# Optimization experiments

Hardware: AMD Instinct MI355X
Metric: run time of the kernel (lower is better)

The kernel has to match this reference:

```python
import jax, jax.numpy as jnp
import numpy as np

B, T, D_MODEL, D_HEAD = 16, 2048, 512, 64
LAMBDA_0 = 1.0      # inverse tracker init: A_0 = I / lambda_0
FIXED_LAMBDA = 1.0  # PenaltyBuilder with fixed_lambda: u_t = sqrt(lambda) * k_t


def setup_inputs() -> dict:
    key = jax.random.key(0)
    ks = jax.random.split(key, 9)
    s_in = 1.0 / np.sqrt(D_MODEL)
    s_out = 1.0 / np.sqrt(D_HEAD)
    return {
        "x": jax.random.normal(ks[0], (B, T, D_MODEL), jnp.float32),
        "W_q": jax.random.normal(ks[1], (D_HEAD, D_MODEL), jnp.float32) * s_in,
        "b_q": jnp.zeros((D_HEAD,), jnp.float32),
        "W_k": jax.random.normal(ks[2], (D_HEAD, D_MODEL), jnp.float32) * s_in,
        "b_k": jnp.zeros((D_HEAD,), jnp.float32),
        "W_v": jax.random.normal(ks[3], (D_HEAD, D_MODEL), jnp.float32) * s_in,
        "b_v": jnp.zeros((D_HEAD,), jnp.float32),
        "W_o": jax.random.normal(ks[4], (D_MODEL, D_HEAD), jnp.float32) * s_out,
        "b_o": jnp.zeros((D_MODEL,), jnp.float32),
    }


def _vla_scan(q, k, v):
    # q,k,v: (B, T, D_HEAD). Sequential recurrence over T with matrix states
    # A_t (Sherman-Morrison inverse of lambda_0*I + sum u u^T) and memory S_t.
    def step(carry, qkv_t):
        A, S = carry                      # (B, d, d) each
        q_t, k_t, v_t = qkv_t             # (B, d) each
        s_t = jnp.sum(k_t * q_t, axis=-1, keepdims=True)   # (B, 1)
        u_t = jnp.sqrt(FIXED_LAMBDA) * k_t                 # penalty direction
        # Sherman-Morrison rank-1 inverse update: A <- A - (A u)(A u)^T / (1 + u^T A u)
        Au = jnp.einsum('bij,bj->bi', A, u_t)              # (B, d)
        denom = 1.0 + jnp.sum(u_t * Au, axis=-1)           # (B,)
        A = A - Au[:, :, None] * Au[:, None, :] / denom[:, None, None]
        # z_t = A_t u_t ; alpha_t = s_t * z_t
        z_t = jnp.einsum('bij,bj->bi', A, u_t)
        alpha_t = s_t * z_t                                # (B, d)
        # memory update: S <- S + v_t alpha_t^T ; output o_t = S q_t
        S = S + v_t[:, :, None] * alpha_t[:, None, :]
        o_t = jnp.einsum('bij,bj->bi', S, q_t)
        return (A, S), o_t

    A0 = jnp.broadcast_to(jnp.eye(D_HEAD, dtype=jnp.float32) / LAMBDA_0,
                          (q.shape[0], D_HEAD, D_HEAD))
    S0 = jnp.zeros((q.shape[0], D_HEAD, D_HEAD), jnp.float32)
    qkv = (q.transpose(1, 0, 2), k.transpose(1, 0, 2), v.transpose(1, 0, 2))  # (T,B,d)
    (_, _), O = jax.lax.scan(step, (A0, S0), qkv)
    return O.transpose(1, 0, 2)  # (B, T, d)


def reference(x, W_q, b_q, W_k, b_k, W_v, b_v, W_o, b_o):
    # Vectorized per-token projections (the torch loop applies them per step)
    q = jnp.einsum('btm,dm->btd', x, W_q) + b_q
    k = jnp.einsum('btm,dm->btd', x, W_k) + b_k
    v = jnp.einsum('btm,dm->btd', x, W_v) + b_v
    O = _vla_scan(q, k, v)
    return jnp.einsum('btd,md->btm', O, W_o) + b_o
```

## Files before the change

kernel.cpp:

```cpp
#include <hip/hip_runtime.h>

#define B_   16
#define T_   2048
#define DM_  512
#define DH_  64
#define NTOK (B_ * T_)

typedef float f32x2 __attribute__((ext_vector_type(2)));
typedef float f32x4 __attribute__((ext_vector_type(4)));

template <int CTRL>
__device__ __forceinline__ float dpp_add_step(float acc) {
    int moved = __builtin_amdgcn_update_dpp(
        0, __builtin_bit_cast(int, acc), CTRL, 0xf, 0xf, true);
    return acc + __builtin_bit_cast(float, moved);
}
__device__ __forceinline__ float wave_sum_bcast(float x) {
    x = dpp_add_step<0x111>(x);
    x = dpp_add_step<0x112>(x);
    x = dpp_add_step<0x114>(x);
    x = dpp_add_step<0x118>(x);
    x = dpp_add_step<0x142>(x);
    x = dpp_add_step<0x143>(x);
    return __builtin_bit_cast(float,
        __builtin_amdgcn_readlane(__builtin_bit_cast(int, x), 63));
}

__global__ __launch_bounds__(256) void proj_kernel(
    const float* __restrict__ x,
    const float* __restrict__ Wq, const float* __restrict__ bq,
    const float* __restrict__ Wk, const float* __restrict__ bk,
    const float* __restrict__ Wv, const float* __restrict__ bvp,
    float* __restrict__ qkv)
{
    __shared__ __align__(16) float xs[32][64];
    __shared__ __align__(16) float ws[32][192];
    const int tid = threadIdx.x;
    const int bt0 = blockIdx.x * 64;
    const int ty  = tid >> 4;
    const int tx  = tid & 15;

    f32x2 acc2[4][6];
#pragma unroll
    for (int i = 0; i < 4; i++)
#pragma unroll
        for (int j = 0; j < 6; j++) acc2[i][j] = (f32x2){0.f, 0.f};

    for (int kb = 0; kb < DM_; kb += 32) {
#pragma unroll
        for (int r = 0; r < 2; r++) {
            int idx = tid + r * 256;
            int tok = idx >> 3, kq = idx & 7;
            f32x4 xv = *(const f32x4*)&x[(size_t)(bt0 + tok) * DM_ + kb + kq * 4];
            xs[kq * 4 + 0][tok] = xv.x;
            xs[kq * 4 + 1][tok] = xv.y;
            xs[kq * 4 + 2][tok] = xv.z;
            xs[kq * 4 + 3][tok] = xv.w;
        }
#pragma unroll
        for (int r = 0; r < 6; r++) {
            int idx = tid + r * 256;
            int d = idx >> 3, kq = idx & 7;
            const float* wrow = (d < 64)  ? (Wq + (size_t)d * DM_)
                              : (d < 128) ? (Wk + (size_t)(d - 64) * DM_)
                                          : (Wv + (size_t)(d - 128) * DM_);
            f32x4 wv4 = *(const f32x4*)&wrow[kb + kq * 4];
            ws[kq * 4 + 0][d] = wv4.x;
            ws[kq * 4 + 1][d] = wv4.y;
            ws[kq * 4 + 2][d] = wv4.z;
            ws[kq * 4 + 3][d] = wv4.w;
        }
        __syncthreads();

#pragma unroll
        for (int kk = 0; kk < 32; kk++) {
            f32x4 x4 = *(const f32x4*)&xs[kk][ty * 4];
            const float xv[4] = {x4.x, x4.y, x4.z, x4.w};
            const f32x2* wsp = (const f32x2*)&ws[kk][tx * 12];
            f32x2 w2[6];
#pragma unroll
            for (int j2 = 0; j2 < 6; j2++) w2[j2] = wsp[j2];
#pragma unroll
            for (int i = 0; i < 4; i++) {
                f32x2 xb = {xv[i], xv[i]};
#pragma unroll
                for (int j2 = 0; j2 < 6; j2++)
                    acc2[i][j2] = __builtin_elementwise_fma(xb, w2[j2], acc2[i][j2]);
            }
        }
        __syncthreads();
    }

#pragma unroll
    for (int i = 0; i < 4; i++) {
        const int bt = bt0 + ty * 4 + i;
        float* dst = qkv + (size_t)bt * 192 + tx * 12;
#pragma unroll
        for (int j2 = 0; j2 < 6; j2++) {
            int c0 = tx * 12 + 2 * j2;
#pragma unroll
            for (int h = 0; h < 2; h++) {
                int c = c0 + h;
                float bias = (c < 64) ? bq[c] : (c < 128) ? bk[c - 64] : bvp[c - 128];
                dst[2 * j2 + h] = ((h == 0) ? acc2[i][j2].x : acc2[i][j2].y) + bias;
            }
        }
    }
}

__global__ __launch_bounds__(256) void sdot_kernel(
    const float* __restrict__ qkv, float* __restrict__ sbuf)
{
    const int tid = blockIdx.x * 256 + threadIdx.x;
    const int tok = tid >> 3, l = tid & 7;
    const float* row = qkv + (size_t)tok * 192 + l * 8;
    f32x4 qa = *(const f32x4*)row;
    f32x4 qb = *(const f32x4*)(row + 4);
    f32x4 ka = *(const f32x4*)(row + 64);
    f32x4 kb = *(const f32x4*)(row + 68);
    float r = qa.x * ka.x + qa.y * ka.y + qa.z * ka.z + qa.w * ka.w
            + qb.x * kb.x + qb.y * kb.y + qb.z * kb.z + qb.w * kb.w;
    r += __shfl_xor(r, 1, 64);
    r += __shfl_xor(r, 2, 64);
    r += __shfl_xor(r, 4, 64);
    if (l == 0) sbuf[tok] = r;
}

__global__ __launch_bounds__(128, 1) void scan_kernel(
    const float* __restrict__ qkv, const float* __restrict__ sbuf,
    float* __restrict__ O)
{
    __shared__ __align__(16) float stage[2][32 * 192];
    __shared__ __align__(16) float sst[2][32];
    __shared__ __align__(16) float au_sm[2][64];
    const int tid  = threadIdx.x;
    const int lane = tid & 63;
    const int w    = tid >> 6;
    const int b    = blockIdx.x;
    const float* src = qkv + (size_t)b * T_ * 192;
    const float* sb  = sbuf + (size_t)b * T_;
    float* Og = O + (size_t)b * T_ * DH_;

    if (w == 1) {
#pragma unroll 2
        for (int r = 0; r < 24; r++)
            *(f32x4*)&stage[0][r * 256 + lane * 4] =
                *(const f32x4*)&src[r * 256 + lane * 4];
        if (lane < 8) ((f32x4*)sst[0])[lane] = ((const f32x4*)sb)[lane];
    } else {
        au_sm[0][lane] = 0.f;
        au_sm[1][lane] = 0.f;
    }
    __syncthreads();

    if (w == 1) {
        for (int blk = 0; blk < 64; ++blk) {
            if (blk + 1 < 64) {
                const float* s2 = src + (size_t)(blk + 1) * 6144;
                float* dst = stage[(blk + 1) & 1];
#pragma unroll 2
                for (int r = 0; r < 24; r++)
                    *(f32x4*)&dst[r * 256 + lane * 4] =
                        *(const f32x4*)&s2[r * 256 + lane * 4];
                if (lane < 8)
                    ((f32x4*)sst[(blk + 1) & 1])[lane] =
                        ((const f32x4*)(sb + (size_t)(blk + 1) * 32))[lane];
            }
            __syncthreads();
        }
    } else {
        f32x2 A2[32], S2[32];
#pragma unroll
        for (int m = 0; m < 32; m++) {
            A2[m].x = (2 * m == lane)     ? 1.f : 0.f;
            A2[m].y = (2 * m + 1 == lane) ? 1.f : 0.f;
            S2[m] = (f32x2){0.f, 0.f};
        }
        float ci = 0.f, vsa = 0.f;

        for (int blk = 0; blk < 64; ++blk) {
            const float* stg = stage[blk & 1];
            const float* ss  = sst[blk & 1];
            float* Ob = Og + (size_t)blk * 32 * DH_;
            for (int tt = 0; tt < 32; ++tt) {
                const float* st = stg + tt * 192;
                const int cb = tt & 1;
                const float* aup = au_sm[cb ^ 1];
                const float ql = st[lane];
                const float kl = st[64 + lane];
                const float vl = st[128 + lane];
                const float s  = ss[tt];
                const f32x2 nci2 = {-ci, -ci};
                const f32x2 vsa2 = {vsa, vsa};

                f32x2 y0 = {0,0}, y1 = {0,0}, y2s = {0,0}, y3 = {0,0};
                f32x2 o0 = {0,0}, o1 = {0,0}, o2s = {0,0}, o3 = {0,0};
#pragma unroll
                for (int jj = 0; jj < 16; jj++) {
                    f32x4 a4 = *(const f32x4*)&aup[jj * 4];
                    f32x4 k4 = *(const f32x4*)&st[64 + jj * 4];
                    f32x4 q4 = *(const f32x4*)&st[jj * 4];
                    f32x2 a2a = {a4.x, a4.y}, a2b = {a4.z, a4.w};
                    f32x2 k2a = {k4.x, k4.y}, k2b = {k4.z, k4.w};
                    f32x2 q2a = {q4.x, q4.y}, q2b = {q4.z, q4.w};
                    A2[2*jj]   = __builtin_elementwise_fma(nci2, a2a, A2[2*jj]);
                    A2[2*jj+1] = __builtin_elementwise_fma(nci2, a2b, A2[2*jj+1]);
                    S2[2*jj]   = __builtin_elementwise_fma(vsa2, a2a, S2[2*jj]);
                    S2[2*jj+1] = __builtin_elementwise_fma(vsa2, a2b, S2[2*jj+1]);
                    if (jj & 1) {
                        y1 = __builtin_elementwise_fma(A2[2*jj],   k2a, y1);
                        y3 = __builtin_elementwise_fma(A2[2*jj+1], k2b, y3);
                        o1 = __builtin_elementwise_fma(S2[2*jj],   q2a, o1);
                        o3 = __builtin_elementwise_fma(S2[2*jj+1], q2b, o3);
                    } else {
                        y0  = __builtin_elementwise_fma(A2[2*jj],   k2a, y0);
                        y2s = __builtin_elementwise_fma(A2[2*jj+1], k2b, y2s);
                        o0  = __builtin_elementwise_fma(S2[2*jj],   q2a, o0);
                        o2s = __builtin_elementwise_fma(S2[2*jj+1], q2b, o2s);
                    }
                }
                f32x2 ys = (y0 + y1) + (y2s + y3);
                const float y = ys.x + ys.y;
                au_sm[cb][lane] = y;

                const float rd = wave_sum_bcast(kl * y);
                const float rq = wave_sum_bcast(ql * y);

                f32x2 os = (o0 + o1) + (o2s + o3);
                const float rinv = __builtin_amdgcn_rcpf(1.0f + rd);
                const float sr = s * rinv;
                Ob[tt * DH_ + lane] = (os.x + os.y) + sr * rq * vl;
                ci  = y * rinv;
                vsa = vl * sr;
            }
            __syncthreads();
        }
    }
}

__global__ __launch_bounds__(256) void oproj_kernel(
    const float* __restrict__ O, const float* __restrict__ Wo,
    const float* __restrict__ bo, float* __restrict__ out)
{
    __shared__ __align__(16) float os[16][64];
    const int tid = threadIdx.x;
    const size_t t0 = (size_t)blockIdx.x * 16;
    {
        int tok = tid >> 4, dq = tid & 15;
        *(f32x4*)&os[tok][dq * 4] = *(const f32x4*)&O[(t0 + tok) * 64 + dq * 4];
    }
    __syncthreads();

    const int m = tid * 2;
    float acc0[16], acc1[16];
#pragma unroll
    for (int i = 0; i < 16; i++) { acc0[i] = 0.f; acc1[i] = 0.f; }

    const float* w0 = Wo + (size_t)m * 64;
    const float* w1 = w0 + 64;
#pragma unroll
    for (int dq = 0; dq < 16; ++dq) {
        f32x4 wa = *(const f32x4*)&w0[dq * 4];
        f32x4 wb = *(const f32x4*)&w1[dq * 4];
#pragma unroll
        for (int tok = 0; tok < 16; ++tok) {
            f32x4 o4 = *(const f32x4*)&os[tok][dq * 4];
            acc0[tok] = fmaf(o4.x, wa.x, fmaf(o4.y, wa.y,
                        fmaf(o4.z, wa.z, fmaf(o4.w, wa.w, acc0[tok]))));
            acc1[tok] = fmaf(o4.x, wb.x, fmaf(o4.y, wb.y,
                        fmaf(o4.z, wb.z, fmaf(o4.w, wb.w, acc1[tok]))));
        }
    }
    const float b0 = bo[m], b1 = bo[m + 1];
#pragma unroll
    for (int tok = 0; tok < 16; ++tok) {
        float2 v = make_float2(acc0[tok] + b0, acc1[tok] + b1);
        *(float2*)&out[(t0 + tok) * DM_ + m] = v;
    }
}

extern "C" void kernel_launch(void* const* d_in, const int* in_sizes, int n_in,
                              void* d_out, int out_size, void* d_ws, size_t ws_size,
                              hipStream_t stream)
{
    const float* x  = (const float*)d_in[0];
    const float* Wq = (const float*)d_in[1];
    const float* bq = (const float*)d_in[2];
    const float* Wk = (const float*)d_in[3];
    const float* bk = (const float*)d_in[4];
    const float* Wv = (const float*)d_in[5];
    const float* bv = (const float*)d_in[6];
    const float* Wo = (const float*)d_in[7];
    const float* bo = (const float*)d_in[8];
    float* out = (float*)d_out;

    float* qkv  = (float*)d_ws;
    float* O    = qkv + (size_t)NTOK * 192;
    float* sbuf = O + (size_t)NTOK * 64;

    proj_kernel<<<NTOK / 64, 256, 0, stream>>>(x, Wq, bq, Wk, bk, Wv, bv, qkv);
    sdot_kernel<<<NTOK * 8 / 256, 256, 0, stream>>>(qkv, sbuf);
    scan_kernel<<<B_, 128, 0, stream>>>(qkv, sbuf, O);
    oproj_kernel<<<NTOK / 16, 256, 0, stream>>>(O, Wo, bo, out);
}
```

Before: 1.590 ms.

## Replace per-token scan with chunked blockwise Sherman-Morrison and memory updates

Rewrites the scan kernel so it processes 32-token chunks. Within each chunk it forms W=A·K and a Gram matrix, then runs a small triangular elimination to apply the 32 rank-1 updates together. Outputs come from an inter-chunk term plus an intra-chunk triangular correction, and A and S are updated once per chunk. This swaps the serial per-token wave reductions for matrix-style work spread across 512 threads per batch. The cost is 32 block barriers per chunk in the elimination loop and a different floating-point ordering.

```diff
diff --git a/kernel.cpp b/kernel.cpp
--- a/kernel.cpp
+++ b/kernel.cpp
@@ -5,6 +5,8 @@
 #define DM_  512
 #define DH_  64
 #define NTOK (B_ * T_)
+#define C_   32
+#define NCH  (T_ / C_)
 
 typedef float f32x2 __attribute__((ext_vector_type(2)));
 typedef float f32x4 __attribute__((ext_vector_type(4)));
@@ -14,16 +16,6 @@
     int moved = __builtin_amdgcn_update_dpp(
         0, __builtin_bit_cast(int, acc), CTRL, 0xf, 0xf, true);
     return acc + __builtin_bit_cast(float, moved);
-}
-__device__ __forceinline__ float wave_sum_bcast(float x) {
-    x = dpp_add_step<0x111>(x);
-    x = dpp_add_step<0x112>(x);
-    x = dpp_add_step<0x114>(x);
-    x = dpp_add_step<0x118>(x);
-    x = dpp_add_step<0x142>(x);
-    x = dpp_add_step<0x143>(x);
-    return __builtin_bit_cast(float,
-        __builtin_amdgcn_readlane(__builtin_bit_cast(int, x), 63));
 }
 
 __global__ __launch_bounds__(256) void proj_kernel(
@@ -126,115 +118,210 @@
     if (l == 0) sbuf[tok] = r;
 }
 
-__global__ __launch_bounds__(128, 1) void scan_kernel(
+__global__ __launch_bounds__(512, 1) void scan_kernel(
     const float* __restrict__ qkv, const float* __restrict__ sbuf,
     float* __restrict__ O)
 {
-    __shared__ __align__(16) float stage[2][32 * 192];
-    __shared__ __align__(16) float sst[2][32];
-    __shared__ __align__(16) float au_sm[2][64];
-    const int tid  = threadIdx.x;
-    const int lane = tid & 63;
-    const int w    = tid >> 6;
-    const int b    = blockIdx.x;
+    __shared__ __align__(16) float A[64][68];
+    __shared__ __align__(16) float KQV[3][32][68];
+    __shared__ __align__(16) float W[32][68];
+    __shared__ __align__(16) float GR[32][36];
+    __shared__ float dv[32], av[32], sv[32];
+
+    const int tid = threadIdx.x;
+    const int b   = blockIdx.x;
     const float* src = qkv + (size_t)b * T_ * 192;
-    const float* sb  = sbuf + (size_t)b * T_;
-    float* Og = O + (size_t)b * T_ * DH_;
-
-    if (w == 1) {
-#pragma unroll 2
-        for (int r = 0; r < 24; r++)
-            *(f32x4*)&stage[0][r * 256 + lane * 4] =
-                *(const f32x4*)&src[r * 256 + lane * 4];
-        if (lane < 8) ((f32x4*)sst[0])[lane] = ((const f32x4*)sb)[lane];
-    } else {
-        au_sm[0][lane] = 0.f;
-        au_sm[1][lane] = 0.f;
+    const float* sbp = sbuf + (size_t)b * T_;
+    float* Og = O + (size_t)b * T_ * 64;
+
+    const int jt  = tid >> 4;
+    const int q16 = tid & 15;
+    const int dow = tid >> 3;
+    const int m0  = (tid & 7) * 8;
+    const int jq  = tid & 7;
+    const int j0q = jq * 4;
+
+    f32x2 sreg[4] = {{0,0},{0,0},{0,0},{0,0}};
+
+    for (int e = tid; e < 64 * 68; e += 512) {
+        int dd = e / 68, mm = e % 68;
+        A[dd][mm] = (dd == mm) ? 1.f : 0.f;
     }
     __syncthreads();
 
-    if (w == 1) {
-        for (int blk = 0; blk < 64; ++blk) {
-            if (blk + 1 < 64) {
-                const float* s2 = src + (size_t)(blk + 1) * 6144;
-                float* dst = stage[(blk + 1) & 1];
-#pragma unroll 2
-                for (int r = 0; r < 24; r++)
-                    *(f32x4*)&dst[r * 256 + lane * 4] =
-                        *(const f32x4*)&s2[r * 256 + lane * 4];
-                if (lane < 8)
-                    ((f32x4*)sst[(blk + 1) & 1])[lane] =
-                        ((const f32x4*)(sb + (size_t)(blk + 1) * 32))[lane];
+    for (int c = 0; c < NCH; ++c) {
+        {
+            const float* s2 = src + (size_t)c * C_ * 192;
+#pragma unroll
+            for (int r = 0; r < 3; r++) {
+                int idx = tid + r * 512;
+                int which = idx >> 9;
+                int t = (idx >> 4) & 31;
+                int dq = (idx & 15) * 4;
+                int off = (which == 0) ? 64 : ((which == 1) ? 0 : 128);
+                *(f32x4*)&KQV[which][t][dq] =
+                    *(const f32x4*)&s2[(size_t)t * 192 + off + dq];
+            }
+            if (tid < 32) sv[tid] = sbp[c * C_ + tid];
+        }
+        __syncthreads();
+
+        float obase[4];
+        {
+            f32x2 wp0 = {0,0}, wp1 = {0,0}, wp2 = {0,0}, wp3 = {0,0};
+#pragma unroll
+            for (int mq = 0; mq < 16; ++mq) {
+                f32x4 kv = *(const f32x4*)&KQV[0][jt][mq * 4];
+                f32x2 k2a = {kv.x, kv.y}, k2b = {kv.z, kv.w};
+                f32x4 a0 = *(const f32x4*)&A[q16     ][mq * 4];
+                f32x4 a1 = *(const f32x4*)&A[q16 + 16][mq * 4];
+                f32x4 a2 = *(const f32x4*)&A[q16 + 32][mq * 4];
+                f32x4 a3 = *(const f32x4*)&A[q16 + 48][mq * 4];
+                wp0 = __builtin_elementwise_fma((f32x2){a0.x,a0.y}, k2a, wp0);
+                wp0 = __builtin_elementwise_fma((f32x2){a0.z,a0.w}, k2b, wp0);
+                wp1 = __builtin_elementwise_fma((f32x2){a1.x,a1.y}, k2a, wp1);
+                wp1 = __builtin_elementwise_fma((f32x2){a1.z,a1.w}, k2b, wp1);
+                wp2 = __builtin_elementwise_fma((f32x2){a2.x,a2.y}, k2a, wp2);
+                wp2 = __builtin_elementwise_fma((f32x2){a2.z,a2.w}, k2b, wp2);
+                wp3 = __builtin_elementwise_fma((f32x2){a3.x,a3.y}, k2a, wp3);
+                wp3 = __builtin_elementwise_fma((f32x2){a3.z,a3.w}, k2b, wp3);
+            }
+            W[jt][q16]      = wp0.x + wp0.y;
+            W[jt][q16 + 16] = wp1.x + wp1.y;
+            W[jt][q16 + 32] = wp2.x + wp2.y;
+            W[jt][q16 + 48] = wp3.x + wp3.y;
+
+            f32x2 part[32];
+#pragma unroll
+            for (int j = 0; j < 32; ++j) part[j] = (f32x2){0.f, 0.f};
+#pragma unroll
+            for (int j = 0; j < 32; ++j) {
+                f32x4 qa = *(const f32x4*)&KQV[1][j][m0];
+                f32x4 qb = *(const f32x4*)&KQV[1][j][m0 + 4];
+                part[j] = __builtin_elementwise_fma(sreg[0], (f32x2){qa.x,qa.y}, part[j]);
+                part[j] = __builtin_elementwise_fma(sreg[1], (f32x2){qa.z,qa.w}, part[j]);
+                part[j] = __builtin_elementwise_fma(sreg[2], (f32x2){qb.x,qb.y}, part[j]);
+                part[j] = __builtin_elementwise_fma(sreg[3], (f32x2){qb.z,qb.w}, part[j]);
+            }
+#pragma unroll
+            for (int j = 0; j < 32; ++j) {
+                float v = part[j].x + part[j].y;
+                v = dpp_add_step<0x141>(v);
+                v = dpp_add_step<0x1B>(v);
+                v = dpp_add_step<0xB1>(v);
+                if ((j >> 2) == jq) obase[j & 3] = v;
+            }
+        }
+        __syncthreads();
+
+        {
+            const int i = jt, jj0 = q16 * 2;
+            f32x2 ga = {0,0}, gb = {0,0};
+#pragma unroll
+            for (int dq = 0; dq < 16; ++dq) {
+                f32x4 w4 = *(const f32x4*)&W[i][dq * 4];
+                f32x4 ka = *(const f32x4*)&KQV[0][jj0][dq * 4];
+                f32x4 kb = *(const f32x4*)&KQV[0][jj0 + 1][dq * 4];
+                ga = __builtin_elementwise_fma((f32x2){w4.x,w4.y}, (f32x2){ka.x,ka.y}, ga);
+                ga = __builtin_elementwise_fma((f32x2){w4.z,w4.w}, (f32x2){ka.z,ka.w}, ga);
+                gb = __builtin_elementwise_fma((f32x2){w4.x,w4.y}, (f32x2){kb.x,kb.y}, gb);
+                gb = __builtin_elementwise_fma((f32x2){w4.z,w4.w}, (f32x2){kb.z,kb.w}, gb);
+            }
+            *(f32x2*)&GR[i][jj0] = (f32x2){ga.x + ga.y, gb.x + gb.y};
+        }
+        __syncthreads();
+
+        for (int t = 0; t < C_; ++t) {
+            const float rd = 1.0f / (1.0f + GR[t][t]);
+            if (tid == 0) { dv[t] = rd; av[t] = sv[t] * rd; }
+            const int j = t + 1 + jt;
+            if (j < 32) {
+                const float mj = GR[t][j] * rd;
+                const int d4 = q16 * 4;
+                f32x4 wt = *(const f32x4*)&W[t][d4];
+                f32x4 wj = *(const f32x4*)&W[j][d4];
+                wj.x -= mj * wt.x; wj.y -= mj * wt.y;
+                wj.z -= mj * wt.z; wj.w -= mj * wt.w;
+                *(f32x4*)&W[j][d4] = wj;
+                if (q16 < 8) {
+                    const int g4 = q16 * 4;
+                    f32x4 gt = *(const f32x4*)&GR[t][g4];
+                    f32x4 gj = *(const f32x4*)&GR[j][g4];
+                    gj.x -= mj * gt.x; gj.y -= mj * gt.y;
+                    gj.z -= mj * gt.z; gj.w -= mj * gt.w;
+                    *(f32x4*)&GR[j][g4] = gj;
+                }
             }
             __syncthreads();
         }
-    } else {
-        f32x2 A2[32], S2[32];
-#pragma unroll
-        for (int m = 0; m < 32; m++) {
-            A2[m].x = (2 * m == lane)     ? 1.f : 0.f;
-            A2[m].y = (2 * m + 1 == lane) ? 1.f : 0.f;
-            S2[m] = (f32x2){0.f, 0.f};
-        }
-        float ci = 0.f, vsa = 0.f;
-
-        for (int blk = 0; blk < 64; ++blk) {
-            const float* stg = stage[blk & 1];
-            const float* ss  = sst[blk & 1];
-            float* Ob = Og + (size_t)blk * 32 * DH_;
-            for (int tt = 0; tt < 32; ++tt) {
-                const float* st = stg + tt * 192;
-                const int cb = tt & 1;
-                const float* aup = au_sm[cb ^ 1];
-                const float ql = st[lane];
-                const float kl = st[64 + lane];
-                const float vl = st[128 + lane];
-                const float s  = ss[tt];
-                const f32x2 nci2 = {-ci, -ci};
-                const f32x2 vsa2 = {vsa, vsa};
-
-                f32x2 y0 = {0,0}, y1 = {0,0}, y2s = {0,0}, y3 = {0,0};
-                f32x2 o0 = {0,0}, o1 = {0,0}, o2s = {0,0}, o3 = {0,0};
-#pragma unroll
-                for (int jj = 0; jj < 16; jj++) {
-                    f32x4 a4 = *(const f32x4*)&aup[jj * 4];
-                    f32x4 k4 = *(const f32x4*)&st[64 + jj * 4];
-                    f32x4 q4 = *(const f32x4*)&st[jj * 4];
-                    f32x2 a2a = {a4.x, a4.y}, a2b = {a4.z, a4.w};
-                    f32x2 k2a = {k4.x, k4.y}, k2b = {k4.z, k4.w};
-                    f32x2 q2a = {q4.x, q4.y}, q2b = {q4.z, q4.w};
-                    A2[2*jj]   = __builtin_elementwise_fma(nci2, a2a, A2[2*jj]);
-                    A2[2*jj+1] = __builtin_elementwise_fma(nci2, a2b, A2[2*jj+1]);
-                    S2[2*jj]   = __builtin_elementwise_fma(vsa2, a2a, S2[2*jj]);
-                    S2[2*jj+1] = __builtin_elementwise_fma(vsa2, a2b, S2[2*jj+1]);
-                    if (jj & 1) {
-                        y1 = __builtin_elementwise_fma(A2[2*jj],   k2a, y1);
-                        y3 = __builtin_elementwise_fma(A2[2*jj+1], k2b, y3);
-                        o1 = __builtin_elementwise_fma(S2[2*jj],   q2a, o1);
-                        o3 = __builtin_elementwise_fma(S2[2*jj+1], q2b, o3);
-                    } else {
-                        y0  = __builtin_elementwise_fma(A2[2*jj],   k2a, y0);
-                        y2s = __builtin_elementwise_fma(A2[2*jj+1], k2b, y2s);
-                        o0  = __builtin_elementwise_fma(S2[2*jj],   q2a, o0);
-                        o2s = __builtin_elementwise_fma(S2[2*jj+1], q2b, o2s);
-                    }
-                }
-                f32x2 ys = (y0 + y1) + (y2s + y3);
-                const float y = ys.x + ys.y;
-                au_sm[cb][lane] = y;
-
-                const float rd = wave_sum_bcast(kl * y);
-                const float rq = wave_sum_bcast(ql * y);
-
-                f32x2 os = (o0 + o1) + (o2s + o3);
-                const float rinv = __builtin_amdgcn_rcpf(1.0f + rd);
-                const float sr = s * rinv;
-                Ob[tt * DH_ + lane] = (os.x + os.y) + sr * rq * vl;
-                ci  = y * rinv;
-                vsa = vl * sr;
-            }
-            __syncthreads();
-        }
+
+        {
+            const int i = jt, jj0 = q16 * 2;
+            f32x2 ra = {0,0}, rb = {0,0};
+#pragma unroll
+            for (int dq = 0; dq < 16; ++dq) {
+                f32x4 w4 = *(const f32x4*)&W[i][dq * 4];
+                f32x4 qa = *(const f32x4*)&KQV[1][jj0][dq * 4];
+                f32x4 qb = *(const f32x4*)&KQV[1][jj0 + 1][dq * 4];
+                ra = __builtin_elementwise_fma((f32x2){w4.x,w4.y}, (f32x2){qa.x,qa.y}, ra);
+                ra = __builtin_elementwise_fma((f32x2){w4.z,w4.w}, (f32x2){qa.z,qa.w}, ra);
+                rb = __builtin_elementwise_fma((f32x2){w4.x,w4.y}, (f32x2){qb.x,qb.y}, rb);
+                rb = __builtin_elementwise_fma((f32x2){w4.z,w4.w}, (f32x2){qb.z,qb.w}, rb);
+            }
+            *(f32x2*)&GR[i][jj0] = (f32x2){ra.x + ra.y, rb.x + rb.y};
+        }
+        __syncthreads();
+
+        {
+            f32x4 oacc = {obase[0], obase[1], obase[2], obase[3]};
+            for (int i = 0; i < j0q; ++i) {
+                const float cv = av[i] * KQV[2][i][dow];
+                f32x4 r4 = *(const f32x4*)&GR[i][j0q];
+                oacc.x += cv * r4.x; oacc.y += cv * r4.y;
+                oacc.z += cv * r4.z; oacc.w += cv * r4.w;
+            }
+            {
+                const float c0 = av[j0q + 0] * KQV[2][j0q + 0][dow];
+                const float c1 = av[j0q + 1] * KQV[2][j0q + 1][dow];
+                const float c2 = av[j0q + 2] * KQV[2][j0q + 2][dow];
+                const float c3 = av[j0q + 3] * KQV[2][j0q + 3][dow];
+                f32x4 r0 = *(const f32x4*)&GR[j0q + 0][j0q];
+                f32x4 r1 = *(const f32x4*)&GR[j0q + 1][j0q];
+                f32x4 r2 = *(const f32x4*)&GR[j0q + 2][j0q];
+                f32x4 r3 = *(const f32x4*)&GR[j0q + 3][j0q];
+                oacc.x += c0 * r0.x;
+                oacc.y += c0 * r0.y + c1 * r1.y;
+                oacc.z += c0 * r0.z + c1 * r1.z + c2 * r2.z;
+                oacc.w += c0 * r0.w + c1 * r1.w + c2 * r2.w + c3 * r3.w;
+            }
+            float* op = &Og[((size_t)c * C_) * 64 + dow];
+            op[(j0q + 0) * 64] = oacc.x;
+            op[(j0q + 1) * 64] = oacc.y;
+            op[(j0q + 2) * 64] = oacc.z;
+            op[(j0q + 3) * 64] = oacc.w;
+        }
+
+        {
+            f32x4 aa0 = *(const f32x4*)&A[dow][m0];
+            f32x4 aa1 = *(const f32x4*)&A[dow][m0 + 4];
+            for (int t = 0; t < C_; ++t) {
+                const float ca = W[t][dow] * dv[t];
+                const float cs = KQV[2][t][dow] * av[t];
+                f32x4 w0 = *(const f32x4*)&W[t][m0];
+                f32x4 w1 = *(const f32x4*)&W[t][m0 + 4];
+                aa0.x -= ca * w0.x; aa0.y -= ca * w0.y;
+                aa0.z -= ca * w0.z; aa0.w -= ca * w0.w;
+                aa1.x -= ca * w1.x; aa1.y -= ca * w1.y;
+                aa1.z -= ca * w1.z; aa1.w -= ca * w1.w;
+                sreg[0] = __builtin_elementwise_fma((f32x2){cs,cs}, (f32x2){w0.x,w0.y}, sreg[0]);
+                sreg[1] = __builtin_elementwise_fma((f32x2){cs,cs}, (f32x2){w0.z,w0.w}, sreg[1]);
+                sreg[2] = __builtin_elementwise_fma((f32x2){cs,cs}, (f32x2){w1.x,w1.y}, sreg[2]);
+                sreg[3] = __builtin_elementwise_fma((f32x2){cs,cs}, (f32x2){w1.z,w1.w}, sreg[3]);
+            }
+            *(f32x4*)&A[dow][m0]     = aa0;
+            *(f32x4*)&A[dow][m0 + 4] = aa1;
+        }
+        __syncthreads();
     }
 }
 
@@ -300,6 +387,6 @@
 
     proj_kernel<<<NTOK / 64, 256, 0, stream>>>(x, Wq, bq, Wk, bk, Wv, bv, qkv);
     sdot_kernel<<<NTOK * 8 / 256, 256, 0, stream>>>(qkv, sbuf);
-    scan_kernel<<<B_, 128, 0, stream>>>(qkv, sbuf, O);
+    scan_kernel<<<B_, 512, 0, stream>>>(qkv, sbuf, O);
     oproj_kernel<<<NTOK / 16, 256, 0, stream>>>(O, Wo, bo, out);
 }
```

Result: faster. 1.457 ms (-8.4%).
